# Kernel optimization log

Measured on AMD Instinct MI355X. Metric: run time of the kernel, lower is better.

The kernel has to match this reference:

```python
import jax, jax.numpy as jnp
import numpy as np

# Static config matching init_kwargs
H = 12            # num_heads
ALPHA = (1, 2, 3)
DEPTH = 5
BLOCK_DEPTH = 3
TOTAL_DEPTH_M1 = 14 - 1   # total_depth - 1
SMALL_ACTIVE = (BLOCK_DEPTH <= DEPTH <= TOTAL_DEPTH_M1 - BLOCK_DEPTH)  # True here


def _ln(x, g, b, eps=1e-5):
    m = jnp.mean(x, axis=-1, keepdims=True)
    v = jnp.mean((x - m) ** 2, axis=-1, keepdims=True)
    return (x - m) * jax.lax.rsqrt(v + eps) * g + b


def _attn_branch(xp, w_qkv, w_proj, b_proj, keep_heads, keep_ch):
    # xp: (B2, N, C). Heads >= keep_heads are zeroed in q,k,v (as in the torch
    # clone+zero), output channels >= keep_ch zeroed after proj.
    B2, N, C = xp.shape
    hd = C // H
    scale = hd ** -0.5
    qkv = (xp @ w_qkv).reshape(B2, N, 3, H, hd).transpose(2, 0, 3, 1, 4)  # (3,B2,H,N,hd)
    hmask = (jnp.arange(H) < keep_heads).astype(xp.dtype)[None, :, None, None]
    q, k, v = qkv[0] * hmask, qkv[1] * hmask, qkv[2] * hmask
    a = jax.nn.softmax(jnp.einsum('bhnd,bhmd->bhnm', q, k) * scale, axis=-1)
    o = jnp.einsum('bhnm,bhmd->bhnd', a, v).transpose(0, 2, 1, 3).reshape(B2, N, C)
    o = o @ w_proj + b_proj
    cmask = (jnp.arange(C) < keep_ch).astype(xp.dtype)
    return o * cmask


def _mlp_branch(xp, w1, b1, w2, b2, keep_ch):
    # Input channels >= keep_ch zeroed before fc1, output channels zeroed after fc2.
    C = xp.shape[-1]
    cmask = (jnp.arange(C) < keep_ch).astype(xp.dtype)
    h = jax.nn.gelu((xp * cmask) @ w1 + b1, approximate=False)  # torch nn.GELU exact
    return ((h @ w2) + b2) * cmask


def setup_inputs() -> dict:
    key = jax.random.key(0)
    ks = jax.random.split(key, 8)
    B, N, C = 64, 257, 768
    HID = 4 * C

    def w(k, shape):
        return jax.random.normal(k, shape, jnp.float32) * 0.02

    return {
        'x': jax.random.normal(ks[0], (B, N, C), jnp.float32),
        'gumbel_weights': jax.random.uniform(ks[1], (3,), jnp.float32),
        'n1l_g': jnp.ones((C,), jnp.float32), 'n1l_b': jnp.zeros((C,), jnp.float32),
        'n1s_g': jnp.ones((C,), jnp.float32), 'n1s_b': jnp.zeros((C,), jnp.float32),
        'w_qkv': w(ks[2], (C, 3 * C)),  # qkv_bias=False
        'w_proj': w(ks[3], (C, C)), 'b_proj': jnp.zeros((C,), jnp.float32),
        'n2l_g': jnp.ones((C,), jnp.float32), 'n2l_b': jnp.zeros((C,), jnp.float32),
        'n2s_g': jnp.ones((C,), jnp.float32), 'n2s_b': jnp.zeros((C,), jnp.float32),
        'w_fc1': w(ks[4], (C, HID)), 'b_fc1': jnp.zeros((HID,), jnp.float32),
        'w_fc2': w(ks[5], (HID, C)), 'b_fc2': jnp.zeros((C,), jnp.float32),
    }


def reference(x, gumbel_weights, n1l_g, n1l_b, n1s_g, n1s_b, w_qkv, w_proj, b_proj,
              n2l_g, n2l_b, n2s_g, n2s_b, w_fc1, b_fc1, w_fc2, b_fc2):
    B, N, C = x.shape
    B2 = B // 2

    # --- attention sub-block (pre-norm, residual) ---
    nl = _ln(x[:B2], n1l_g, n1l_b)
    ns = _ln(x[B2:], n1s_g, n1s_b)
    a_large = _attn_branch(nl, w_qkv, w_proj, b_proj, H, C)
    if SMALL_ACTIVE:
        a_small = sum(
            gumbel_weights[i] * _attn_branch(ns, w_qkv, w_proj, b_proj,
                                             H // ALPHA[i], C // ALPHA[i])
            for i in range(3))
        attn_out = jnp.concatenate([a_large, a_small], axis=0)
    else:
        attn_out = jnp.concatenate([a_large, a_large], axis=0)
    x = x + attn_out  # drop_path = Identity

    # --- mlp sub-block (pre-norm, residual) ---
    nl2 = _ln(x[:B2], n2l_g, n2l_b)
    ns2 = _ln(x[B2:], n2s_g, n2s_b)
    m_large = _mlp_branch(nl2, w_fc1, b_fc1, w_fc2, b_fc2, C)
    if SMALL_ACTIVE:
        m_small = sum(
            gumbel_weights[i] * _mlp_branch(ns2, w_fc1, b_fc1, w_fc2, b_fc2,
                                            C // ALPHA[i])
            for i in range(3))
        mlp_out = jnp.concatenate([m_large, m_small], axis=0)
    else:
        mlp_out = jnp.concatenate([m_large, m_large], axis=0)
    return x + mlp_out
```

## Files before the change

### kernel.cpp

```cpp
#include <hip/hip_runtime.h>
#include <hip/hip_bf16.h>

typedef short v8s __attribute__((ext_vector_type(8)));
typedef short v4s __attribute__((ext_vector_type(4)));
typedef float v4f __attribute__((ext_vector_type(4)));

#define B2ROWS 8224
#define ROWS   16448

__device__ __forceinline__ float fast_gelu(float z) {
  float u = z * 0.70710678118654752f;
  float a = fabsf(u);
  float t = __builtin_amdgcn_rcpf(1.0f + 0.3275911f * a);
  float p = t * (0.254829592f + t * (-0.284496736f + t * (1.421413741f +
            t * (-1.453152027f + t * 1.061405429f))));
  float e = __expf(-a * a);
  float erfa = 1.0f - p * e;
  float erfu = copysignf(erfa, u);
  return 0.5f * z * (1.0f + erfu);
}

__global__ __launch_bounds__(256) void wprep(const float* __restrict__ W,
                                             __hip_bfloat16* __restrict__ Wt,
                                             int K, int N, int variant,
                                             const float* __restrict__ gw) {
  int k = blockIdx.x * 256 + threadIdx.x;
  int n = blockIdx.y;
  if (k >= K) return;
  float v = W[(size_t)k * N + n];
  if (variant == 1) {
    int h = k >> 6;
    float s = gw[0];
    if (h < 6 && n < 384) s += gw[1];
    if (h < 4 && n < 256) s += gw[2];
    v *= s;
  }
  Wt[(size_t)n * K + k] = __float2bfloat16(v);
}

__global__ void bias_prep(const float* __restrict__ bp, const float* __restrict__ b2,
                          const float* __restrict__ gw,
                          float* __restrict__ b_small, float* __restrict__ b2_small) {
  int c = blockIdx.x * 256 + threadIdx.x;
  if (c >= 768) return;
  float s = gw[0] + (c < 384 ? gw[1] : 0.f) + (c < 256 ? gw[2] : 0.f);
  b_small[c] = bp[c] * s;
  b2_small[c] = b2[c] * s;
}

__global__ __launch_bounds__(256) void ln_k(const float* __restrict__ X,
                                            __hip_bfloat16* __restrict__ out,
                                            const float* __restrict__ gl, const float* __restrict__ bl,
                                            const float* __restrict__ gs, const float* __restrict__ bs) {
  int wave = threadIdx.x >> 6, lane = threadIdx.x & 63;
  int row = blockIdx.x * 4 + wave;
  const float* g = (row < B2ROWS) ? gl : gs;
  const float* b = (row < B2ROWS) ? bl : bs;
  const float* xr = X + (size_t)row * 768;
  float v[12]; float s = 0.f, ss = 0.f;
#pragma unroll
  for (int i = 0; i < 12; i++) { v[i] = xr[lane + i * 64]; s += v[i]; ss += v[i] * v[i]; }
#pragma unroll
  for (int o = 32; o > 0; o >>= 1) { s += __shfl_xor(s, o, 64); ss += __shfl_xor(ss, o, 64); }
  float mean = s * (1.0f / 768.0f);
  float var = ss * (1.0f / 768.0f) - mean * mean;
  float rstd = rsqrtf(var + 1e-5f);
  __hip_bfloat16* orow = out + (size_t)row * 768;
#pragma unroll
  for (int i = 0; i < 12; i++) {
    int c = lane + i * 64;
    orow[c] = __float2bfloat16((v[i] - mean) * rstd * g[c] + b[c]);
  }
}

__global__ __launch_bounds__(256) void gemm_k(
    const __hip_bfloat16* __restrict__ A, int lda,
    const __hip_bfloat16* __restrict__ Bt, int ldb,
    int M, int K,
    const float* __restrict__ bias,
    const float* __restrict__ resid, int ldr,
    const float* __restrict__ gw, int gidx,
    const __hip_bfloat16* __restrict__ addin,
    void* __restrict__ out, int ldo,
    int mode,
    const __hip_bfloat16* __restrict__ aux1,
    const __hip_bfloat16* __restrict__ aux2,
    const float* __restrict__ bias2) {
  __shared__ __attribute__((aligned(16))) short Asm[3][128 * 32];
  __shared__ __attribute__((aligned(16))) short Bsm[3][128 * 32];
  int tid = threadIdx.x;
  int lane = tid & 63;
  int wave = tid >> 6;
  int wm = wave >> 1, wn = wave & 1;
  int l16 = lane & 15, quad = lane >> 4;

  int gx = gridDim.x;
  int nwg = gx * gridDim.y;
  int bid = blockIdx.y * gx + blockIdx.x;
  int q8 = nwg >> 3, r8 = nwg & 7;
  int xcd = bid & 7, lid = bid >> 3;
  int nb = (xcd < r8 ? xcd * (q8 + 1) : r8 * (q8 + 1) + (xcd - r8) * q8) + lid;
  int m0 = (nb / gx) * 128, n0 = (nb % gx) * 128;

  int sw = (quad ^ ((l16 >> 1) & 3)) * 8;

  const __hip_bfloat16* Ause = A;
  const __hip_bfloat16* Btuse = Bt;
  const float* bias_u = bias;
  const float* resid_u = resid;
  void* out_u = out;
  if (mode == 4) {
    if (n0 < 256) Ause = aux2;
    else if (n0 < 384) Ause = aux1;
    mode = 2;
  } else if (mode == 5) {
    if (m0 >= 8320) {
      m0 -= 8320;
      Ause = A + (size_t)B2ROWS * lda;
      Btuse = aux1;
      bias_u = bias2;
      resid_u = resid + (size_t)B2ROWS * ldr;
      out_u = (void*)((float*)out + (size_t)B2ROWS * ldo);
    }
    mode = 2;
  }

  int r4 = lane >> 2;
  int qs = (lane & 3) ^ ((r4 >> 1) & 3);

  const ushort* Au = (const ushort*)Ause;
  const ushort* Bu = (const ushort*)Btuse;

  const ushort* agp[2];
  const ushort* bgp[2];
  int lof[2];
#pragma unroll
  for (int it = 0; it < 2; it++) {
    int rbase = wave * 16 + it * 64;
    int gr = m0 + rbase + r4; if (gr > M - 1) gr = M - 1;
    agp[it] = Au + (size_t)gr * lda + qs * 8;
    int gn = n0 + rbase + r4;
    bgp[it] = Bu + (size_t)gn * ldb + qs * 8;
    lof[it] = rbase * 32;
  }

  v4f acc[4][4];
#pragma unroll
  for (int i = 0; i < 4; i++)
#pragma unroll
    for (int j = 0; j < 4; j++) acc[i][j] = (v4f){0.f, 0.f, 0.f, 0.f};

  auto stage = [&](int buf, int ko) {
#pragma unroll
    for (int it = 0; it < 2; it++) {
      __builtin_amdgcn_global_load_lds(
          (const __attribute__((address_space(1))) uint32_t*)(uintptr_t)(const void*)(agp[it] + ko),
          (__attribute__((address_space(3))) uint32_t*)(uint32_t)(uintptr_t)(const void*)&Asm[buf][lof[it]],
          16, 0, 0);
      __builtin_amdgcn_global_load_lds(
          (const __attribute__((address_space(1))) uint32_t*)(uintptr_t)(const void*)(bgp[it] + ko),
          (__attribute__((address_space(3))) uint32_t*)(uint32_t)(uintptr_t)(const void*)&Bsm[buf][lof[it]],
          16, 0, 0);
    }
  };

  int nk = K >> 5;
  stage(0, 0);
  stage(1, 32);

  int bc = 0;
  for (int t = 0; t < nk; ++t) {
    __builtin_amdgcn_sched_barrier(0);
    if (t + 1 < nk) {
      asm volatile("s_waitcnt vmcnt(4)" ::: "memory");
    } else {
      asm volatile("s_waitcnt vmcnt(0)" ::: "memory");
    }
    __builtin_amdgcn_s_barrier();
    __builtin_amdgcn_sched_barrier(0);
    if (t + 2 < nk) {
      int bsg = bc - 1; if (bsg < 0) bsg += 3;
      stage(bsg, (t + 2) * 32);
    }
    v8s af[4], bfr[4];
#pragma unroll
    for (int i = 0; i < 4; i++) af[i] = *(const v8s*)&Asm[bc][(wm * 64 + i * 16 + l16) * 32 + sw];
#pragma unroll
    for (int j = 0; j < 4; j++) bfr[j] = *(const v8s*)&Bsm[bc][(wn * 64 + j * 16 + l16) * 32 + sw];
#pragma unroll
    for (int i = 0; i < 4; i++)
#pragma unroll
      for (int j = 0; j < 4; j++)
        acc[i][j] = __builtin_amdgcn_mfma_f32_16x16x32_bf16(af[i], bfr[j], acc[i][j], 0, 0, 0);
    bc++; if (bc == 3) bc = 0;
  }

  float scale = (gidx >= 0) ? gw[gidx] : 1.0f;

  __syncthreads();
  char* sbase = ((wave < 2) ? (char*)Asm : (char*)Bsm) + (wave & 1) * 12288;

  if (mode != 2) {
    ushort* S16 = (ushort*)sbase;
#pragma unroll
    for (int i = 0; i < 4; i++) {
#pragma unroll
      for (int j = 0; j < 4; j++) {
        int gc = n0 + wn * 64 + j * 16 + l16;
#pragma unroll
        for (int r = 0; r < 4; r++) {
          float v = acc[i][j][r];
          if (mode == 1) {
            float z = v + bias_u[gc];
            v = scale * fast_gelu(z);
          }
          __hip_bfloat16 hb = __float2bfloat16(v);
          S16[(i * 16 + quad * 4 + r) * 72 + j * 16 + l16] = *(const ushort*)&hb;
        }
      }
    }
    asm volatile("s_waitcnt lgkmcnt(0)" ::: "memory");
#pragma unroll
    for (int rr = 0; rr < 8; rr++) {
      int row = rr * 8 + (lane >> 3);
      int col0 = (lane & 7) * 8;
      int gr = m0 + wm * 64 + row;
      v8s val = *(const v8s*)&S16[row * 72 + col0];
      if (gr < M) {
        size_t go = (size_t)gr * ldo + (n0 + wn * 64 + col0);
        if (mode == 1 && addin) {
          v8s av = *(const v8s*)&((const ushort*)addin)[go];
#pragma unroll
          for (int e = 0; e < 8; e++) {
            float fv = __uint_as_float(((uint)(ushort)val[e]) << 16);
            float fa = __uint_as_float(((uint)(ushort)av[e]) << 16);
            __hip_bfloat16 hr = __float2bfloat16(fv + fa);
            val[e] = *(const short*)&hr;
          }
        }
        *(v8s*)&((ushort*)out_u)[go] = val;
      }
    }
  } else {
    float* S32 = (float*)sbase;
#pragma unroll
    for (int h = 0; h < 2; h++) {
      if (h) asm volatile("s_waitcnt lgkmcnt(0)" ::: "memory");
#pragma unroll
      for (int i = 0; i < 4; i++) {
#pragma unroll
        for (int jj = 0; jj < 2; jj++) {
          int j = h * 2 + jj;
          int gc = n0 + wn * 64 + j * 16 + l16;
#pragma unroll
          for (int r = 0; r < 4; r++)
            S32[(i * 16 + quad * 4 + r) * 36 + jj * 16 + l16] = acc[i][j][r] + bias_u[gc];
        }
      }
      asm volatile("s_waitcnt lgkmcnt(0)" ::: "memory");
#pragma unroll
      for (int rr = 0; rr < 8; rr++) {
        int row = rr * 8 + (lane >> 3);
        int c0 = (lane & 7) * 4;
        int gr = m0 + wm * 64 + row;
        v4f v = *(const v4f*)&S32[row * 36 + c0];
        if (gr < M) {
          int gc0 = n0 + wn * 64 + h * 32 + c0;
          v4f rv = *(const v4f*)&resid_u[(size_t)gr * ldr + gc0];
          v4f sres = v + rv;
          *(v4f*)&((float*)out_u)[(size_t)gr * ldo + gc0] = sres;
        }
      }
    }
  }
}

__global__ __launch_bounds__(256) void fc1f_k(
    const __hip_bfloat16* __restrict__ A, int lda,
    const __hip_bfloat16* __restrict__ Bt, int ldb,
    int M, int K,
    const float* __restrict__ bias,
    const float* __restrict__ gw,
    void* __restrict__ out, int ldo,
    __hip_bfloat16* __restrict__ outB,
    __hip_bfloat16* __restrict__ outC) {
  __shared__ __attribute__((aligned(16))) short As2[3][128 * 32];
  __shared__ __attribute__((aligned(16))) short Bs2[3][64 * 32];
  int tid = threadIdx.x, lane = tid & 63, wave = tid >> 6;
  int wm = wave >> 1, wn = wave & 1;
  int l16 = lane & 15, quad = lane >> 4;

  int gx = gridDim.x;
  int nwg = gx * gridDim.y;
  int bid = blockIdx.y * gx + blockIdx.x;
  int q8 = nwg >> 3, r8 = nwg & 7;
  int xcd = bid & 7, lid = bid >> 3;
  int nb = (xcd < r8 ? xcd * (q8 + 1) : r8 * (q8 + 1) + (xcd - r8) * q8) + lid;
  int m0 = (nb / gx) * 128, n0 = (nb % gx) * 64;

  int sw = (quad ^ ((l16 >> 1) & 3)) * 8;
  int r4 = lane >> 2;
  int qs = (lane & 3) ^ ((r4 >> 1) & 3);

  const ushort* Au = (const ushort*)A;
  const ushort* Bu = (const ushort*)Bt;
  const ushort* agp[2];
#pragma unroll
  for (int it = 0; it < 2; it++) {
    int gr = m0 + wave * 16 + it * 64 + r4; if (gr > M - 1) gr = M - 1;
    agp[it] = Au + (size_t)gr * lda + qs * 8;
  }
  const ushort* bgp = Bu + (size_t)(n0 + wave * 16 + r4) * ldb + qs * 8;

  v4f acc[4][2];
#pragma unroll
  for (int i = 0; i < 4; i++)
#pragma unroll
    for (int j = 0; j < 2; j++) acc[i][j] = (v4f){0.f, 0.f, 0.f, 0.f};

  float gw0 = gw[0], gw1 = gw[1], gw2 = gw[2];
  float bias2r[2];
#pragma unroll
  for (int j = 0; j < 2; j++) bias2r[j] = bias[n0 + wn * 32 + j * 16 + l16];

  uint g1p[4][2][2], g2p[4][2][2];

  auto snap = [&](uint (&gp)[4][2][2], float gwX) {
#pragma unroll
    for (int i = 0; i < 4; i++)
#pragma unroll
      for (int j = 0; j < 2; j++)
#pragma unroll
        for (int p = 0; p < 2; p++) {
          float v0 = gwX * fast_gelu(acc[i][j][2 * p] + bias2r[j]);
          float v1 = gwX * fast_gelu(acc[i][j][2 * p + 1] + bias2r[j]);
          __hip_bfloat16 h0 = __float2bfloat16(v0);
          __hip_bfloat16 h1 = __float2bfloat16(v1);
          gp[i][j][p] = ((uint)*(const ushort*)&h1 << 16) | (uint)*(const ushort*)&h0;
        }
  };

  auto stage = [&](int buf, int ko) {
#pragma unroll
    for (int it = 0; it < 2; it++) {
      __builtin_amdgcn_global_load_lds(
          (const __attribute__((address_space(1))) uint32_t*)(uintptr_t)(const void*)(agp[it] + ko),
          (__attribute__((address_space(3))) uint32_t*)(uint32_t)(uintptr_t)(const void*)&As2[buf][(wave * 16 + it * 64) * 32],
          16, 0, 0);
    }
    __builtin_amdgcn_global_load_lds(
        (const __attribute__((address_space(1))) uint32_t*)(uintptr_t)(const void*)(bgp + ko),
        (__attribute__((address_space(3))) uint32_t*)(uint32_t)(uintptr_t)(const void*)&Bs2[buf][(wave * 16) * 32],
        16, 0, 0);
  };

  int nk = K >> 5;
  stage(0, 0);
  stage(1, 32);

  int bc = 0;
  for (int t = 0; t < nk; ++t) {
    if (t == 8)  snap(g2p, gw2);
    if (t == 12) snap(g1p, gw1);
    __builtin_amdgcn_sched_barrier(0);
    if (t + 1 < nk) {
      asm volatile("s_waitcnt vmcnt(3)" ::: "memory");
    } else {
      asm volatile("s_waitcnt vmcnt(0)" ::: "memory");
    }
    __builtin_amdgcn_s_barrier();
    __builtin_amdgcn_sched_barrier(0);
    if (t + 2 < nk) {
      int bsg = bc - 1; if (bsg < 0) bsg += 3;
      stage(bsg, (t + 2) * 32);
    }
    v8s af[4], bfr[2];
#pragma unroll
    for (int i = 0; i < 4; i++) af[i] = *(const v8s*)&As2[bc][(wm * 64 + i * 16 + l16) * 32 + sw];
#pragma unroll
    for (int j = 0; j < 2; j++) bfr[j] = *(const v8s*)&Bs2[bc][(wn * 32 + j * 16 + l16) * 32 + sw];
#pragma unroll
    for (int i = 0; i < 4; i++)
#pragma unroll
      for (int j = 0; j < 2; j++)
        acc[i][j] = __builtin_amdgcn_mfma_f32_16x16x32_bf16(af[i], bfr[j], acc[i][j], 0, 0, 0);
    bc++; if (bc == 3) bc = 0;
  }

#pragma unroll
  for (int i = 0; i < 4; i++)
#pragma unroll
    for (int j = 0; j < 2; j++)
#pragma unroll
      for (int r = 0; r < 4; r++)
        acc[i][j][r] = gw0 * fast_gelu(acc[i][j][r] + bias2r[j]);

  __syncthreads();
  ushort* S = (ushort*)As2 + wave * 2560;

  auto flush = [&](void* dst) {
    asm volatile("s_waitcnt lgkmcnt(0)" ::: "memory");
#pragma unroll
    for (int i = 0; i < 4; i++)
#pragma unroll
      for (int j = 0; j < 2; j++)
#pragma unroll
        for (int r = 0; r < 4; r++) {
          __hip_bfloat16 hb = __float2bfloat16(acc[i][j][r]);
          S[(i * 16 + quad * 4 + r) * 40 + j * 16 + l16] = *(const ushort*)&hb;
        }
    asm volatile("s_waitcnt lgkmcnt(0)" ::: "memory");
#pragma unroll
    for (int rr = 0; rr < 8; rr++) {
      int row = rr * 8 + (lane >> 3);
      int col0 = (lane & 7) * 4;
      int gr = m0 + wm * 64 + row;
      v4s val = *(const v4s*)&S[row * 40 + col0];
      if (gr < M)
        *(v4s*)&((ushort*)dst)[(size_t)gr * ldo + (n0 + wn * 32 + col0)] = val;
    }
  };

  flush(out);
#pragma unroll
  for (int i = 0; i < 4; i++)
#pragma unroll
    for (int j = 0; j < 2; j++)
#pragma unroll
      for (int p = 0; p < 2; p++) {
        uint u = g1p[i][j][p];
        acc[i][j][2 * p]     += __uint_as_float(u << 16);
        acc[i][j][2 * p + 1] += __uint_as_float(u & 0xffff0000u);
      }
  flush(outB);
#pragma unroll
  for (int i = 0; i < 4; i++)
#pragma unroll
    for (int j = 0; j < 2; j++)
#pragma unroll
      for (int p = 0; p < 2; p++) {
        uint u = g2p[i][j][p];
        acc[i][j][2 * p]     += __uint_as_float(u << 16);
        acc[i][j][2 * p + 1] += __uint_as_float(u & 0xffff0000u);
      }
  flush(outC);
}

__global__ __launch_bounds__(256) void attn_k(const __hip_bfloat16* __restrict__ qkv,
                                              __hip_bfloat16* __restrict__ O) {
  __shared__ ushort Ks[64 * 72];
  __shared__ ushort Vs[64 * 64];
  __shared__ ushort Ps[4][16 * 72];
  int bh = blockIdx.x;
  int b = bh / 12, h = bh % 12;
  size_t base = (size_t)b * 257;
  const ushort* Qg = (const ushort*)qkv;
  int tid = threadIdx.x;
  int w = tid >> 6, lane = tid & 63;
  int l16 = lane & 15, quad = lane >> 4;
  int qrow0 = blockIdx.y * 64 + w * 16;

  v8s aq[2];
  {
    int gr = qrow0 + l16; if (gr > 256) gr = 256;
    const ushort* qp = Qg + (base + gr) * 2304 + h * 64;
    aq[0] = *(const v8s*)(qp + quad * 8);
    aq[1] = *(const v8s*)(qp + 32 + quad * 8);
  }

  float mrow[4], lrow[4];
  v4f o[4];
#pragma unroll
  for (int r = 0; r < 4; r++) { mrow[r] = -1e30f; lrow[r] = 0.f; }
#pragma unroll
  for (int dt = 0; dt < 4; dt++) o[dt] = (v4f){0.f, 0.f, 0.f, 0.f};

  for (int kt = 0; kt < 5; kt++) {
    __syncthreads();
#pragma unroll
    for (int it = 0; it < 2; it++) {
      int ch = tid + it * 256;
      int row = ch >> 3, oct = ch & 7;
      int gk = kt * 64 + row; if (gk > 256) gk = 256;
      *(uint4*)&Ks[row * 72 + oct * 8] =
        *(const uint4*)(Qg + (base + gk) * 2304 + 768 + h * 64 + oct * 8);
    }
#pragma unroll
    for (int it = 0; it < 2; it++) {
      int oct = w + it * 4;
      int gk = kt * 64 + lane; if (gk > 256) gk = 256;
      ushort tmp[8];
      *(uint4*)tmp = *(const uint4*)(Qg + (base + gk) * 2304 + 1536 + h * 64 + oct * 8);
#pragma unroll
      for (int j = 0; j < 8; j++) {
        int d = oct * 8 + j;
        Vs[d * 64 + (((lane >> 3) ^ j) * 8) + (lane & 7)] = tmp[j];
      }
    }
    __syncthreads();

    v4f s[4];
#pragma unroll
    for (int jt = 0; jt < 4; jt++) {
      v8s bk0 = *(const v8s*)&Ks[(jt * 16 + l16) * 72 + quad * 8];
      v8s bk1 = *(const v8s*)&Ks[(jt * 16 + l16) * 72 + 32 + quad * 8];
      v4f acc = (v4f){0.f, 0.f, 0.f, 0.f};
      acc = __builtin_amdgcn_mfma_f32_16x16x32_bf16(aq[0], bk0, acc, 0, 0, 0);
      acc = __builtin_amdgcn_mfma_f32_16x16x32_bf16(aq[1], bk1, acc, 0, 0, 0);
      s[jt] = acc;
    }
#pragma unroll
    for (int jt = 0; jt < 4; jt++) {
      int col = kt * 64 + jt * 16 + l16;
      bool valid = col < 257;
#pragma unroll
      for (int r = 0; r < 4; r++)
        s[jt][r] = valid ? s[jt][r] * 0.125f : -1e30f;
    }
    float mnew[4], alpha[4], psum[4];
#pragma unroll
    for (int r = 0; r < 4; r++) {
      float mx = fmaxf(fmaxf(s[0][r], s[1][r]), fmaxf(s[2][r], s[3][r]));
#pragma unroll
      for (int off = 1; off < 16; off <<= 1) mx = fmaxf(mx, __shfl_xor(mx, off, 64));
      mnew[r] = fmaxf(mrow[r], mx);
      alpha[r] = __expf(mrow[r] - mnew[r]);
      mrow[r] = mnew[r];
      psum[r] = 0.f;
    }
#pragma unroll
    for (int jt = 0; jt < 4; jt++) {
#pragma unroll
      for (int r = 0; r < 4; r++) {
        float p = __expf(s[jt][r] - mnew[r]);
        psum[r] += p;
        __hip_bfloat16 pb = __float2bfloat16(p);
        Ps[w][(quad * 4 + r) * 72 + jt * 16 + l16] = *(ushort*)&pb;
      }
    }
#pragma unroll
    for (int r = 0; r < 4; r++) {
#pragma unroll
      for (int off = 1; off < 16; off <<= 1) psum[r] += __shfl_xor(psum[r], off, 64);
      lrow[r] = lrow[r] * alpha[r] + psum[r];
    }
#pragma unroll
    for (int dt = 0; dt < 4; dt++)
#pragma unroll
      for (int r = 0; r < 4; r++) o[dt][r] *= alpha[r];
    v8s pa0 = *(const v8s*)&Ps[w][l16 * 72 + quad * 8];
    v8s pa1 = *(const v8s*)&Ps[w][l16 * 72 + 32 + quad * 8];
#pragma unroll
    for (int dt = 0; dt < 4; dt++) {
      int d = dt * 16 + l16;
      v8s bv0 = *(const v8s*)&Vs[d * 64 + ((quad ^ (d & 7)) * 8)];
      v8s bv1 = *(const v8s*)&Vs[d * 64 + (((4 + quad) ^ (d & 7)) * 8)];
      o[dt] = __builtin_amdgcn_mfma_f32_16x16x32_bf16(pa0, bv0, o[dt], 0, 0, 0);
      o[dt] = __builtin_amdgcn_mfma_f32_16x16x32_bf16(pa1, bv1, o[dt], 0, 0, 0);
    }
  }
#pragma unroll
  for (int r = 0; r < 4; r++) {
    int gr = qrow0 + quad * 4 + r;
    if (gr < 257) {
      float inv = 1.f / lrow[r];
      __hip_bfloat16* orow = O + (base + gr) * 768 + h * 64;
#pragma unroll
      for (int dt = 0; dt < 4; dt++)
        orow[dt * 16 + l16] = __float2bfloat16(o[dt][r] * inv);
    }
  }
}

extern "C" void kernel_launch(void* const* d_in, const int* in_sizes, int n_in,
                              void* d_out, int out_size, void* d_ws, size_t ws_size,
                              hipStream_t stream) {
  const float* x      = (const float*)d_in[0];
  const float* gw     = (const float*)d_in[1];
  const float* n1l_g  = (const float*)d_in[2];
  const float* n1l_b  = (const float*)d_in[3];
  const float* n1s_g  = (const float*)d_in[4];
  const float* n1s_b  = (const float*)d_in[5];
  const float* w_qkv  = (const float*)d_in[6];
  const float* w_proj = (const float*)d_in[7];
  const float* b_proj = (const float*)d_in[8];
  const float* n2l_g  = (const float*)d_in[9];
  const float* n2l_b  = (const float*)d_in[10];
  const float* n2s_g  = (const float*)d_in[11];
  const float* n2s_b  = (const float*)d_in[12];
  const float* w_fc1  = (const float*)d_in[13];
  const float* b_fc1  = (const float*)d_in[14];
  const float* w_fc2  = (const float*)d_in[15];
  const float* b_fc2  = (const float*)d_in[16];
  float* out = (float*)d_out;

  const size_t REQUIRED = (size_t)(2304*768 + 2*768*768 + 2*3072*768) * 2
                        + 2 * 768 * 4 + 512
                        + (size_t)ROWS * 768 * 2
                        + (size_t)ROWS * 2304 * 2;
  if (ws_size < REQUIRED) return;

  char* ws = (char*)d_ws;
  size_t off = 0;
  auto alloc = [&](size_t bytes) -> void* {
    void* p = ws + off;
    off = (off + bytes + 255) & ~(size_t)255;
    return p;
  };
  __hip_bfloat16* wqkv_t  = (__hip_bfloat16*)alloc((size_t)2304 * 768 * 2);
  __hip_bfloat16* wproj_l = (__hip_bfloat16*)alloc((size_t)768 * 768 * 2);
  __hip_bfloat16* wproj_s = (__hip_bfloat16*)alloc((size_t)768 * 768 * 2);
  __hip_bfloat16* wfc1_t  = (__hip_bfloat16*)alloc((size_t)3072 * 768 * 2);
  __hip_bfloat16* wfc2_t  = (__hip_bfloat16*)alloc((size_t)768 * 3072 * 2);
  float* b_small  = (float*)alloc(768 * 4);
  float* b2_small = (float*)alloc(768 * 4);
  __hip_bfloat16* xn   = (__hip_bfloat16*)alloc((size_t)ROWS * 768 * 2);
  __hip_bfloat16* qkv  = (__hip_bfloat16*)alloc((size_t)ROWS * 2304 * 2);
  __hip_bfloat16* Obuf = xn;
  __hip_bfloat16* xn2  = qkv;
  __hip_bfloat16* hbuf = qkv + (size_t)ROWS * 768;

  const size_t HB2 = (size_t)B2ROWS * 3072 * 2;
  bool roomy = ws_size >= REQUIRED + 2 * HB2 + 512;
  __hip_bfloat16 *outB = nullptr, *outC = nullptr;
  if (roomy) {
    outB = (__hip_bfloat16*)alloc(HB2);
    outC = (__hip_bfloat16*)alloc(HB2);
  }

  wprep<<<dim3(3, 2304), 256, 0, stream>>>(w_qkv, wqkv_t, 768, 2304, 0, gw);
  wprep<<<dim3(3, 768),  256, 0, stream>>>(w_proj, wproj_l, 768, 768, 0, gw);
  wprep<<<dim3(3, 768),  256, 0, stream>>>(w_proj, wproj_s, 768, 768, 1, gw);
  wprep<<<dim3(3, 3072), 256, 0, stream>>>(w_fc1, wfc1_t, 768, 3072, 0, gw);
  wprep<<<dim3(12, 768), 256, 0, stream>>>(w_fc2, wfc2_t, 3072, 768, 0, gw);
  bias_prep<<<3, 256, 0, stream>>>(b_proj, b_fc2, gw, b_small, b2_small);

  ln_k<<<ROWS / 4, 256, 0, stream>>>(x, xn, n1l_g, n1l_b, n1s_g, n1s_b);

  gemm_k<<<dim3(18, 129), 256, 0, stream>>>(xn, 768, wqkv_t, 768, ROWS, 768,
                                            nullptr, nullptr, 0, gw, -1, nullptr,
                                            qkv, 2304, 0, nullptr, nullptr, nullptr);
  attn_k<<<dim3(768, 5), 256, 0, stream>>>(qkv, Obuf);

  gemm_k<<<dim3(6, 130), 256, 0, stream>>>(Obuf, 768, wproj_l, 768, B2ROWS, 768,
                                           b_proj, x, 768, gw, -1, nullptr, out, 768, 5,
                                           wproj_s, nullptr, b_small);

  ln_k<<<ROWS / 4, 256, 0, stream>>>(out, xn2, n2l_g, n2l_b, n2s_g, n2s_b);
  const __hip_bfloat16* xn2s = xn2 + (size_t)B2ROWS * 768;
  float* outs = out + (size_t)B2ROWS * 768;

  gemm_k<<<dim3(24, 65), 256, 0, stream>>>(xn2, 768, wfc1_t, 768, B2ROWS, 768,
                                           b_fc1, nullptr, 0, gw, -1, nullptr, hbuf, 3072, 1,
                                           nullptr, nullptr, nullptr);
  gemm_k<<<dim3(6, 65), 256, 0, stream>>>(hbuf, 3072, wfc2_t, 3072, B2ROWS, 3072,
                                          b_fc2, out, 768, gw, -1, nullptr, out, 768, 2,
                                          nullptr, nullptr, nullptr);

  if (roomy) {
    fc1f_k<<<dim3(48, 65), 256, 0, stream>>>(xn2s, 768, wfc1_t, 768, B2ROWS, 768,
                                             b_fc1, gw, hbuf, 3072, outB, outC);
    gemm_k<<<dim3(6, 65), 256, 0, stream>>>(hbuf, 3072, wfc2_t, 3072, B2ROWS, 3072,
                                            b2_small, outs, 768, gw, -1, nullptr, outs, 768, 4,
                                            outB, outC, nullptr);
  } else {
    gemm_k<<<dim3(24, 65), 256, 0, stream>>>(xn2s, 768, wfc1_t, 768, B2ROWS, 768,
                                             b_fc1, nullptr, 0, gw, 0, nullptr, hbuf, 3072, 1,
                                             nullptr, nullptr, nullptr);
    gemm_k<<<dim3(3, 65), 256, 0, stream>>>(hbuf, 3072, wfc2_t + (size_t)384 * 3072, 3072, B2ROWS, 3072,
                                            b2_small + 384, outs + 384, 768, gw, -1, nullptr, outs + 384, 768, 2,
                                            nullptr, nullptr, nullptr);
    gemm_k<<<dim3(24, 65), 256, 0, stream>>>(xn2s, 768, wfc1_t, 768, B2ROWS, 384,
                                             b_fc1, nullptr, 0, gw, 1, hbuf, hbuf, 3072, 1,
                                             nullptr, nullptr, nullptr);
    gemm_k<<<dim3(1, 65), 256, 0, stream>>>(hbuf, 3072, wfc2_t + (size_t)256 * 3072, 3072, B2ROWS, 3072,
                                            b2_small + 256, outs + 256, 768, gw, -1, nullptr, outs + 256, 768, 2,
                                            nullptr, nullptr, nullptr);
    gemm_k<<<dim3(24, 65), 256, 0, stream>>>(xn2s, 768, wfc1_t, 768, B2ROWS, 256,
                                             b_fc1, nullptr, 0, gw, 2, hbuf, hbuf, 3072, 1,
                                             nullptr, nullptr, nullptr);
    gemm_k<<<dim3(2, 65), 256, 0, stream>>>(hbuf, 3072, wfc2_t, 3072, B2ROWS, 3072,
                                            b2_small, outs, 768, gw, -1, nullptr, outs, 768, 2,
                                            nullptr, nullptr, nullptr);
  }
}
```

Measured before the change: 726.6 us.

## Merge large and small FC1/FC2 MLP launches into single combined grids

Adds an fc1m_k kernel that runs the large-half and small-half FC1 GEMMs in one 130-row-tile launch. Small-half tiles snapshot GELU partials at the K=256 and K=384 boundaries and write three bf16 hidden buffers. A new gemm_k mode 6 then does both FC2 halves in one launch, choosing the A buffer by output column range. This removes two kernel launches and the tail underutilisation of separate half-size grids, at the cost of an extra workspace buffer and more hidden-state traffic.

```diff
diff --git a/kernel.cpp b/kernel.cpp
--- a/kernel.cpp
+++ b/kernel.cpp
@@ -85,7 +85,8 @@
     int mode,
     const __hip_bfloat16* __restrict__ aux1,
     const __hip_bfloat16* __restrict__ aux2,
-    const float* __restrict__ bias2) {
+    const float* __restrict__ bias2,
+    const __hip_bfloat16* __restrict__ aux3) {
   __shared__ __attribute__((aligned(16))) short Asm[3][128 * 32];
   __shared__ __attribute__((aligned(16))) short Bsm[3][128 * 32];
   int tid = threadIdx.x;
@@ -123,6 +124,17 @@
       out_u = (void*)((float*)out + (size_t)B2ROWS * ldo);
     }
     mode = 2;
+  } else if (mode == 6) {
+    if (m0 >= 8320) {
+      m0 -= 8320;
+      if (n0 < 256) Ause = aux2;
+      else if (n0 < 384) Ause = aux1;
+      else Ause = aux3;
+      bias_u = bias2;
+      resid_u = resid + (size_t)B2ROWS * ldr;
+      out_u = (void*)((float*)out + (size_t)B2ROWS * ldo);
+    }
+    mode = 2;
   }
 
   int r4 = lane >> 2;
@@ -273,6 +285,189 @@
       }
     }
   }
+}
+
+__global__ __launch_bounds__(256) void fc1m_k(
+    const __hip_bfloat16* __restrict__ A, int lda,
+    const __hip_bfloat16* __restrict__ Bt, int ldb,
+    int M, int K,
+    const float* __restrict__ bias,
+    const float* __restrict__ gw,
+    __hip_bfloat16* __restrict__ outL,
+    __hip_bfloat16* __restrict__ out0,
+    __hip_bfloat16* __restrict__ outB,
+    __hip_bfloat16* __restrict__ outC,
+    int ldo) {
+  __shared__ __attribute__((aligned(16))) short As2[3][128 * 32];
+  __shared__ __attribute__((aligned(16))) short Bs2[3][64 * 32];
+  int tid = threadIdx.x, lane = tid & 63, wave = tid >> 6;
+  int wm = wave >> 1, wn = wave & 1;
+  int l16 = lane & 15, quad = lane >> 4;
+
+  int gx = gridDim.x;
+  int nwg = gx * gridDim.y;
+  int bid = blockIdx.y * gx + blockIdx.x;
+  int q8 = nwg >> 3, r8 = nwg & 7;
+  int xcd = bid & 7, lid = bid >> 3;
+  int nb = (xcd < r8 ? xcd * (q8 + 1) : r8 * (q8 + 1) + (xcd - r8) * q8) + lid;
+  int mt = nb / gx;
+  bool sm = (mt >= 65);
+  int m0 = (sm ? mt - 65 : mt) * 128;
+  int n0 = (nb % gx) * 64;
+
+  int sw = (quad ^ ((l16 >> 1) & 3)) * 8;
+  int r4 = lane >> 2;
+  int qs = (lane & 3) ^ ((r4 >> 1) & 3);
+
+  const ushort* Au = (const ushort*)A + (sm ? (size_t)B2ROWS * lda : 0);
+  const ushort* Bu = (const ushort*)Bt;
+  const ushort* agp[2];
+#pragma unroll
+  for (int it = 0; it < 2; it++) {
+    int gr = m0 + wave * 16 + it * 64 + r4; if (gr > M - 1) gr = M - 1;
+    agp[it] = Au + (size_t)gr * lda + qs * 8;
+  }
+  const ushort* bgp = Bu + (size_t)(n0 + wave * 16 + r4) * ldb + qs * 8;
+
+  v4f acc[4][2];
+#pragma unroll
+  for (int i = 0; i < 4; i++)
+#pragma unroll
+    for (int j = 0; j < 2; j++) acc[i][j] = (v4f){0.f, 0.f, 0.f, 0.f};
+
+  float gw0 = gw[0], gw1 = gw[1], gw2 = gw[2];
+  float bias2r[2];
+#pragma unroll
+  for (int j = 0; j < 2; j++) bias2r[j] = bias[n0 + wn * 32 + j * 16 + l16];
+
+  uint g1p[4][2][2], g2p[4][2][2];
+
+  auto snap = [&](uint (&gp)[4][2][2], float gwX) {
+#pragma unroll
+    for (int i = 0; i < 4; i++)
+#pragma unroll
+      for (int j = 0; j < 2; j++)
+#pragma unroll
+        for (int p = 0; p < 2; p++) {
+          float v0 = gwX * fast_gelu(acc[i][j][2 * p] + bias2r[j]);
+          float v1 = gwX * fast_gelu(acc[i][j][2 * p + 1] + bias2r[j]);
+          __hip_bfloat16 h0 = __float2bfloat16(v0);
+          __hip_bfloat16 h1 = __float2bfloat16(v1);
+          gp[i][j][p] = ((uint)*(const ushort*)&h1 << 16) | (uint)*(const ushort*)&h0;
+        }
+  };
+
+  auto stage = [&](int buf, int ko) {
+#pragma unroll
+    for (int it = 0; it < 2; it++) {
+      __builtin_amdgcn_global_load_lds(
+          (const __attribute__((address_space(1))) uint32_t*)(uintptr_t)(const void*)(agp[it] + ko),
+          (__attribute__((address_space(3))) uint32_t*)(uint32_t)(uintptr_t)(const void*)&As2[buf][(wave * 16 + it * 64) * 32],
+          16, 0, 0);
+    }
+    __builtin_amdgcn_global_load_lds(
+        (const __attribute__((address_space(1))) uint32_t*)(uintptr_t)(const void*)(bgp + ko),
+        (__attribute__((address_space(3))) uint32_t*)(uint32_t)(uintptr_t)(const void*)&Bs2[buf][(wave * 16) * 32],
+        16, 0, 0);
+  };
+
+  int nk = K >> 5;
+  stage(0, 0);
+  stage(1, 32);
+
+  int bc = 0;
+  for (int t = 0; t < nk; ++t) {
+    if (sm) {
+      if (t == 8)  snap(g2p, gw2);
+      if (t == 12) snap(g1p, gw1);
+    }
+    __builtin_amdgcn_sched_barrier(0);
+    if (t + 1 < nk) {
+      asm volatile("s_waitcnt vmcnt(3)" ::: "memory");
+    } else {
+      asm volatile("s_waitcnt vmcnt(0)" ::: "memory");
+    }
+    __builtin_amdgcn_s_barrier();
+    __builtin_amdgcn_sched_barrier(0);
+    if (t + 2 < nk) {
+      int bsg = bc - 1; if (bsg < 0) bsg += 3;
+      stage(bsg, (t + 2) * 32);
+    }
+    v8s af[4], bfr[2];
+#pragma unroll
+    for (int i = 0; i < 4; i++) af[i] = *(const v8s*)&As2[bc][(wm * 64 + i * 16 + l16) * 32 + sw];
+#pragma unroll
+    for (int j = 0; j < 2; j++) bfr[j] = *(const v8s*)&Bs2[bc][(wn * 32 + j * 16 + l16) * 32 + sw];
+#pragma unroll
+    for (int i = 0; i < 4; i++)
+#pragma unroll
+      for (int j = 0; j < 2; j++)
+        acc[i][j] = __builtin_amdgcn_mfma_f32_16x16x32_bf16(af[i], bfr[j], acc[i][j], 0, 0, 0);
+    bc++; if (bc == 3) bc = 0;
+  }
+
+  float s0 = sm ? gw0 : 1.0f;
+#pragma unroll
+  for (int i = 0; i < 4; i++)
+#pragma unroll
+    for (int j = 0; j < 2; j++)
+#pragma unroll
+      for (int r = 0; r < 4; r++)
+        acc[i][j][r] = s0 * fast_gelu(acc[i][j][r] + bias2r[j]);
+
+  __syncthreads();
+  ushort* S = (ushort*)As2 + wave * 2560;
+
+  auto flush = [&](void* dst) {
+    asm volatile("s_waitcnt lgkmcnt(0)" ::: "memory");
+#pragma unroll
+    for (int i = 0; i < 4; i++)
+#pragma unroll
+      for (int j = 0; j < 2; j++)
+#pragma unroll
+        for (int r = 0; r < 4; r++) {
+          __hip_bfloat16 hb = __float2bfloat16(acc[i][j][r]);
+          S[(i * 16 + quad * 4 + r) * 40 + j * 16 + l16] = *(const ushort*)&hb;
+        }
+    asm volatile("s_waitcnt lgkmcnt(0)" ::: "memory");
+#pragma unroll
+    for (int rr = 0; rr < 8; rr++) {
+      int row = rr * 8 + (lane >> 3);
+      int col0 = (lane & 7) * 4;
+      int gr = m0 + wm * 64 + row;
+      v4s val = *(const v4s*)&S[row * 40 + col0];
+      if (gr < M)
+        *(v4s*)&((ushort*)dst)[(size_t)gr * ldo + (n0 + wn * 32 + col0)] = val;
+    }
+  };
+
+  if (!sm) {
+    flush(outL);
+    return;
+  }
+  flush(out0);
+#pragma unroll
+  for (int i = 0; i < 4; i++)
+#pragma unroll
+    for (int j = 0; j < 2; j++)
+#pragma unroll
+      for (int p = 0; p < 2; p++) {
+        uint u = g1p[i][j][p];
+        acc[i][j][2 * p]     += __uint_as_float(u << 16);
+        acc[i][j][2 * p + 1] += __uint_as_float(u & 0xffff0000u);
+      }
+  flush(outB);
+#pragma unroll
+  for (int i = 0; i < 4; i++)
+#pragma unroll
+    for (int j = 0; j < 2; j++)
+#pragma unroll
+      for (int p = 0; p < 2; p++) {
+        uint u = g2p[i][j][p];
+        acc[i][j][2 * p]     += __uint_as_float(u << 16);
+        acc[i][j][2 * p + 1] += __uint_as_float(u & 0xffff0000u);
+      }
+  flush(outC);
 }
 
 __global__ __launch_bounds__(256) void fc1f_k(
@@ -621,9 +816,14 @@
   __hip_bfloat16* hbuf = qkv + (size_t)ROWS * 768;
 
   const size_t HB2 = (size_t)B2ROWS * 3072 * 2;
-  bool roomy = ws_size >= REQUIRED + 2 * HB2 + 512;
-  __hip_bfloat16 *outB = nullptr, *outC = nullptr;
-  if (roomy) {
+  bool roomy3 = ws_size >= REQUIRED + 3 * HB2 + 1024;
+  bool roomy2 = ws_size >= REQUIRED + 2 * HB2 + 512;
+  __hip_bfloat16 *outB = nullptr, *outC = nullptr, *g0s = nullptr;
+  if (roomy3) {
+    outB = (__hip_bfloat16*)alloc(HB2);
+    outC = (__hip_bfloat16*)alloc(HB2);
+    g0s  = (__hip_bfloat16*)alloc(HB2);
+  } else if (roomy2) {
     outB = (__hip_bfloat16*)alloc(HB2);
     outC = (__hip_bfloat16*)alloc(HB2);
   }
@@ -639,48 +839,59 @@
 
   gemm_k<<<dim3(18, 129), 256, 0, stream>>>(xn, 768, wqkv_t, 768, ROWS, 768,
                                             nullptr, nullptr, 0, gw, -1, nullptr,
-                                            qkv, 2304, 0, nullptr, nullptr, nullptr);
+                                            qkv, 2304, 0, nullptr, nullptr, nullptr, nullptr);
   attn_k<<<dim3(768, 5), 256, 0, stream>>>(qkv, Obuf);
 
   gemm_k<<<dim3(6, 130), 256, 0, stream>>>(Obuf, 768, wproj_l, 768, B2ROWS, 768,
                                            b_proj, x, 768, gw, -1, nullptr, out, 768, 5,
-                                           wproj_s, nullptr, b_small);
+                                           wproj_s, nullptr, b_small, nullptr);
 
   ln_k<<<ROWS / 4, 256, 0, stream>>>(out, xn2, n2l_g, n2l_b, n2s_g, n2s_b);
   const __hip_bfloat16* xn2s = xn2 + (size_t)B2ROWS * 768;
   float* outs = out + (size_t)B2ROWS * 768;
 
-  gemm_k<<<dim3(24, 65), 256, 0, stream>>>(xn2, 768, wfc1_t, 768, B2ROWS, 768,
-                                           b_fc1, nullptr, 0, gw, -1, nullptr, hbuf, 3072, 1,
-                                           nullptr, nullptr, nullptr);
-  gemm_k<<<dim3(6, 65), 256, 0, stream>>>(hbuf, 3072, wfc2_t, 3072, B2ROWS, 3072,
-                                          b_fc2, out, 768, gw, -1, nullptr, out, 768, 2,
-                                          nullptr, nullptr, nullptr);
-
-  if (roomy) {
+  if (roomy3) {
+    fc1m_k<<<dim3(48, 130), 256, 0, stream>>>(xn2, 768, wfc1_t, 768, B2ROWS, 768,
+                                              b_fc1, gw, hbuf, g0s, outB, outC, 3072);
+    gemm_k<<<dim3(6, 130), 256, 0, stream>>>(hbuf, 3072, wfc2_t, 3072, B2ROWS, 3072,
+                                             b_fc2, out, 768, gw, -1, nullptr, out, 768, 6,
+                                             outB, outC, b2_small, g0s);
+  } else if (roomy2) {
+    gemm_k<<<dim3(24, 65), 256, 0, stream>>>(xn2, 768, wfc1_t, 768, B2ROWS, 768,
+                                             b_fc1, nullptr, 0, gw, -1, nullptr, hbuf, 3072, 1,
+                                             nullptr, nullptr, nullptr, nullptr);
+    gemm_k<<<dim3(6, 65), 256, 0, stream>>>(hbuf, 3072, wfc2_t, 3072, B2ROWS, 3072,
+                                            b_fc2, out, 768, gw, -1, nullptr, out, 768, 2,
+                                            nullptr, nullptr, nullptr, nullptr);
     fc1f_k<<<dim3(48, 65), 256, 0, stream>>>(xn2s, 768, wfc1_t, 768, B2ROWS, 768,
                                              b_fc1, gw, hbuf, 3072, outB, outC);
     gemm_k<<<dim3(6, 65), 256, 0, stream>>>(hbuf, 3072, wfc2_t, 3072, B2ROWS, 3072,
                                             b2_small, outs, 768, gw, -1, nullptr, outs, 768, 4,
-                                            outB, outC, nullptr);
+                                            outB, outC, nullptr, nullptr);
   } else {
+    gemm_k<<<dim3(24, 65), 256, 0, stream>>>(xn2, 768, wfc1_t, 768, B2ROWS, 768,
+                                             b_fc1, nullptr, 0, gw, -1, nullptr, hbuf, 3072, 1,
+                                             nullptr, nullptr, nullptr, nullptr);
+    gemm_k<<<dim3(6, 65), 256, 0, stream>>>(hbuf, 3072, wfc2_t, 3072, B2ROWS, 3072,
+                                            b_fc2, out, 768, gw, -1, nullptr, out, 768, 2,
+                                            nullptr, nullptr, nullptr, nullptr);
     gemm_k<<<dim3(24, 65), 256, 0, stream>>>(xn2s, 768, wfc1_t, 768, B2ROWS, 768,
                                              b_fc1, nullptr, 0, gw, 0, nullptr, hbuf, 3072, 1,
-                                             nullptr, nullptr, nullptr);
+                                             nullptr, nullptr, nullptr, nullptr);
     gemm_k<<<dim3(3, 65), 256, 0, stream>>>(hbuf, 3072, wfc2_t + (size_t)384 * 3072, 3072, B2ROWS, 3072,
                                             b2_small + 384, outs + 384, 768, gw, -1, nullptr, outs + 384, 768, 2,
-                                            nullptr, nullptr, nullptr);
+                                            nullptr, nullptr, nullptr, nullptr);
     gemm_k<<<dim3(24, 65), 256, 0, stream>>>(xn2s, 768, wfc1_t, 768, B2ROWS, 384,
                                              b_fc1, nullptr, 0, gw, 1, hbuf, hbuf, 3072, 1,
-                                             nullptr, nullptr, nullptr);
+                                             nullptr, nullptr, nullptr, nullptr);
     gemm_k<<<dim3(1, 65), 256, 0, stream>>>(hbuf, 3072, wfc2_t + (size_t)256 * 3072, 3072, B2ROWS, 3072,
                                             b2_small + 256, outs + 256, 768, gw, -1, nullptr, outs + 256, 768, 2,
-                                            nullptr, nullptr, nullptr);
+                                            nullptr, nullptr, nullptr, nullptr);
     gemm_k<<<dim3(24, 65), 256, 0, stream>>>(xn2s, 768, wfc1_t, 768, B2ROWS, 256,
                                              b_fc1, nullptr, 0, gw, 2, hbuf, hbuf, 3072, 1,
-                                             nullptr, nullptr, nullptr);
+                                             nullptr, nullptr, nullptr, nullptr);
     gemm_k<<<dim3(2, 65), 256, 0, stream>>>(hbuf, 3072, wfc2_t, 3072, B2ROWS, 3072,
                                             b2_small, outs, 768, gw, -1, nullptr, outs, 768, 2,
-                                            nullptr, nullptr, nullptr);
+                                            nullptr, nullptr, nullptr, nullptr);
   }
 }
```

After: 758.4 us. 1.04x slower.
